# Kernel tuning notes

Hardware: AMD Instinct MI355X
Metric: run time of the kernel (lower is better)

## Reference

```python
import math
import jax, jax.numpy as jnp
import numpy as np

L, B = 576, 16           # residues, batch
HID, ALPHA = 800, 60     # lstm hidden, alphabet size
IN0, IN1 = 41, 2 * HID   # lstm layer input sizes (20 one-hot + 21 pssm)


def _unit(v):
    return v / jnp.linalg.norm(v, axis=-1, keepdims=True)


def _frame(a, b, c):
    # rotation matrix (columns) of the local reference frame at point c
    bc = _unit(c - b)
    n = _unit(jnp.cross(b - a, bc))
    return jnp.stack([bc, jnp.cross(n, bc), n], axis=-1)  # (..., 3, 3)


def _extend(a, b, c, ct):
    # place next atom given previous three atoms and SRF coordinates ct
    R = _frame(a, b, c)
    return c + jnp.einsum('...ij,...j->...i', R, ct)


def lstm_dir(x, w_ih, w_hh, b_ih, b_hh, reverse=False):
    # single-direction LSTM over x: (T, B, D); torch gate order i,f,g,o
    H = w_hh.shape[1]
    Bb = x.shape[1]

    def step(carry, xt):
        h, cst = carry
        gates = xt @ w_ih.T + b_ih + h @ w_hh.T + b_hh
        i, f, g, o = jnp.split(gates, 4, axis=-1)
        cnew = jax.nn.sigmoid(f) * cst + jax.nn.sigmoid(i) * jnp.tanh(g)
        hnew = jax.nn.sigmoid(o) * jnp.tanh(cnew)
        return (hnew, cnew), hnew

    zeros = jnp.zeros((Bb, H), x.dtype)
    _, hs = jax.lax.scan(step, (zeros, zeros), x, reverse=reverse)
    return hs  # (T, B, H), in original time order for both directions


def torsion_to_srf(r, theta, phi):
    # r, theta: (3,) fixed bond lengths/angles; phi: (L, B, 3) torsions
    r = r[None, None, :]
    th = theta[None, None, :]
    c = jnp.stack([r * jnp.cos(th) * jnp.ones_like(phi),
                   r * jnp.cos(phi) * jnp.sin(th),
                   r * jnp.sin(phi) * jnp.sin(th)], axis=-1)  # (L, B, 3, 3)
    Lx, Bx = phi.shape[0], phi.shape[1]
    return jnp.transpose(c, (0, 2, 1, 3)).reshape(3 * Lx, Bx, 3)


def pnerf(c_tilde, nfrag):
    # parallel NeRF: run nfrag fragments in parallel, then stitch sequentially
    A, Bb, _ = c_tilde.shape
    F = A // nfrag  # assumes divisibility (guaranteed by chosen L)
    c = c_tilde.reshape(nfrag, F, Bb, 3).transpose(1, 0, 2, 3).reshape(F, nfrag * Bb, 3)
    init = jnp.array([[-np.sqrt(0.5), np.sqrt(1.5), 0.0],
                      [-np.sqrt(2.0), 0.0, 0.0],
                      [0.0, 0.0, 0.0]], dtype=c_tilde.dtype)
    a0 = jnp.broadcast_to(init[0], (nfrag * Bb, 3))
    b0 = jnp.broadcast_to(init[1], (nfrag * Bb, 3))
    c0 = jnp.broadcast_to(init[2], (nfrag * Bb, 3))

    def step(carry, ct):
        a, b, cc = carry
        d = _extend(a, b, cc, ct)
        return (b, cc, d), d

    _, frag = jax.lax.scan(step, (a0, b0, c0), c)  # (F, nfrag*Bb, 3)
    frag = frag.reshape(F, nfrag, Bb, 3)

    coords = frag[:, 0]  # fragment 0 already in global frame
    for k in range(1, nfrag):  # small fixed loop over fragments
        R = _frame(coords[-3], coords[-2], coords[-1])  # (Bb, 3, 3)
        g = coords[-1][None] + jnp.einsum('bij,fbj->fbi', R, frag[:, k])
        coords = jnp.concatenate([coords, g], axis=0)
    return coords  # (3L, B, 3)


def _p(k, shape):
    return 0.05 * jax.random.normal(k, shape, dtype=jnp.float32)


def setup_inputs():
    key = jax.random.key(0)
    ks = jax.random.split(key, 32)
    inp = {}
    inp['seq'] = jax.random.randint(ks[0], (L, B), 0, 20)
    inp['pssm'] = jax.random.uniform(ks[1], (L, B, 21), dtype=jnp.float32)
    inp['length'] = jnp.full((B,), L, dtype=jnp.int32)  # full lengths (packing is a no-op)
    i = 2
    for layer, din in ((0, IN0), (1, IN1)):
        for d in ('f', 'b'):
            inp[f'w_ih_l{layer}{d}'] = _p(ks[i], (4 * HID, din)); i += 1
            inp[f'w_hh_l{layer}{d}'] = _p(ks[i], (4 * HID, HID)); i += 1
            inp[f'b_ih_l{layer}{d}'] = _p(ks[i], (4 * HID,)); i += 1
            inp[f'b_hh_l{layer}{d}'] = _p(ks[i], (4 * HID,)); i += 1
    inp['fc_w'] = _p(ks[i], (ALPHA, 2 * HID)); i += 1
    inp['fc_b'] = _p(ks[i], (ALPHA,)); i += 1
    inp['alphabet'] = jax.random.uniform(ks[i], (ALPHA, 3), minval=-math.pi, maxval=math.pi, dtype=jnp.float32); i += 1
    inp['bond_lengths'] = jnp.array([145.867432, 152.534744, 132.935516], dtype=jnp.float32)
    inp['bond_angles'] = jnp.array([1.019982, 1.20471, 1.109421], dtype=jnp.float32)
    return inp


def reference(seq, pssm, length,
              w_ih_l0f, w_hh_l0f, b_ih_l0f, b_hh_l0f,
              w_ih_l0b, w_hh_l0b, b_ih_l0b, b_hh_l0b,
              w_ih_l1f, w_hh_l1f, b_ih_l1f, b_hh_l1f,
              w_ih_l1b, w_hh_l1b, b_ih_l1b, b_hh_l1b,
              fc_w, fc_b, alphabet, bond_lengths, bond_angles):
    # eval mode: inter-layer dropout omitted; all lengths == L so packing is identity
    x = jnp.concatenate([jax.nn.one_hot(seq, 20, dtype=pssm.dtype), pssm], axis=-1)  # (L,B,41)
    h = jnp.concatenate([lstm_dir(x, w_ih_l0f, w_hh_l0f, b_ih_l0f, b_hh_l0f),
                         lstm_dir(x, w_ih_l0b, w_hh_l0b, b_ih_l0b, b_hh_l0b, reverse=True)], axis=-1)
    h = jnp.concatenate([lstm_dir(h, w_ih_l1f, w_hh_l1f, b_ih_l1f, b_hh_l1f),
                         lstm_dir(h, w_ih_l1b, w_hh_l1b, b_ih_l1b, b_hh_l1b, reverse=True)], axis=-1)
    p = jax.nn.softmax(h @ fc_w.T + fc_b, axis=-1)            # (L,B,ALPHA)
    phi = jnp.arctan2(p @ jnp.sin(alphabet), p @ jnp.cos(alphabet))  # (L,B,3)
    srf = torsion_to_srf(bond_lengths, bond_angles, phi)      # (3L,B,3)
    return pnerf(srf, int(math.sqrt(L)))                      # (3L,B,3)
```

## Files before the change

kernel.cpp:

```cpp
#include <hip/hip_runtime.h>
#include <hip/hip_fp16.h>

#define L_SEQ 576
#define BATCH 16
#define HIDDEN 800
#define NT 200
#define KQ_HH 25
#define KQ_L1 50
#define KQ_L0 2

typedef _Float16 h8 __attribute__((ext_vector_type(8)));
typedef _Float16 h4 __attribute__((ext_vector_type(4)));
typedef float f4 __attribute__((ext_vector_type(4)));
typedef int v4i __attribute__((ext_vector_type(4)));
typedef int v2i __attribute__((ext_vector_type(2)));

__device__ __forceinline__ float sigmoidf_(float x){
  x = fminf(30.f, fmaxf(-30.f, x));
  return 1.f/(1.f+__expf(-x));
}
__device__ __forceinline__ float tanhf_(float x){
  x = fminf(15.f, fmaxf(-15.f, x));
  float e = __expf(2.f*x);
  return (e-1.f)/(e+1.f);
}

__global__ void init_h(v4i* __restrict__ h){
  size_t i = (size_t)blockIdx.x*256 + threadIdx.x;
  v4i s = {0x7C007C00, 0x7C007C00, 0x7C007C00, 0x7C007C00};
  h[i] = s;
}

__global__ void build_x(const int* __restrict__ seq, const float* __restrict__ pssm,
                        _Float16* __restrict__ x){
  int i = blockIdx.x*256 + threadIdx.x;
  if(i >= L_SEQ*BATCH*64) return;
  int m = i >> 6, k = i & 63;
  float v = 0.f;
  if(k < 20)      v = (seq[m]==k) ? 1.f : 0.f;
  else if(k < 41) v = pssm[m*21 + (k-20)];
  x[i] = (_Float16)v;
}

__global__ void prep_w(
  const float* __restrict__ whh0f, const float* __restrict__ whh0b,
  const float* __restrict__ whh1f, const float* __restrict__ whh1b,
  const float* __restrict__ wih1f, const float* __restrict__ wih1b,
  const float* __restrict__ wih0f, const float* __restrict__ wih0b,
  h8* __restrict__ wp_hh, h8* __restrict__ wp1, h8* __restrict__ wp0)
{
  long idx = (long)blockIdx.x*256 + threadIdx.x;
  const long J1 = 4L*320000, J2 = 2L*640000, J3 = 2L*25600;
  if(idx < J1){
    int d = (int)(idx/320000); int r = (int)(idx%320000);
    int T = r/1600, q = (r%1600)/64, l = r&63;
    const float* W = (d==0)?whh0f:(d==1)?whh0b:(d==2)?whh1f:whh1b;
    int c = l&15; int n = (c&3)*800 + T*4 + (c>>2);
    const float* src = W + (size_t)n*800 + q*32 + ((l>>4)<<3);
    h8 v;
    #pragma unroll
    for(int j=0;j<8;++j) v[j] = (_Float16)src[j];
    wp_hh[idx] = v;
  } else if(idx < J1+J2){
    long i2 = idx - J1;
    int d = (int)(i2/640000); int r = (int)(i2%640000);
    int T = r/3200, q = (r%3200)/64, l = r&63;
    const float* W = d ? wih1b : wih1f;
    int c = l&15; int n = (c&3)*800 + T*4 + (c>>2);
    const float* src = W + (size_t)n*1600 + q*32 + ((l>>4)<<3);
    h8 v;
    #pragma unroll
    for(int j=0;j<8;++j) v[j] = (_Float16)src[j];
    wp1[i2] = v;
  } else if(idx < J1+J2+J3){
    long i3 = idx - J1 - J2;
    int d = (int)(i3/25600); int r = (int)(i3%25600);
    int T = r/128, q = (r%128)/64, l = r&63;
    const float* W = d ? wih0b : wih0f;
    int c = l&15; int n = (c&3)*800 + T*4 + (c>>2);
    int k0 = q*32 + ((l>>4)<<3);
    h8 v;
    #pragma unroll
    for(int j=0;j<8;++j){ int k = k0+j; v[j] = (_Float16)((k<41)? W[(size_t)n*41+k] : 0.f); }
    wp0[i3] = v;
  }
}

__global__ __launch_bounds__(256) void gemm_l0(
  const _Float16* __restrict__ A,
  const h8* __restrict__ WpF, const h8* __restrict__ WpB,
  const float* __restrict__ bihF, const float* __restrict__ bhhF,
  const float* __restrict__ bihB, const float* __restrict__ bhhB,
  _Float16* __restrict__ GpF, _Float16* __restrict__ GpB)
{
  const int wv = threadIdx.x >> 6;
  const int l  = threadIdx.x & 63;
  const int mg = blockIdx.x % 144;
  const int tg = blockIdx.x / 144;
  const int mt = mg*4 + wv;
  const int dir = tg / 50;
  const int Tb  = (tg % 50) * 4;
  const h8* Wp = dir ? WpB : WpF;
  const float* bih = dir ? bihB : bihF;
  const float* bhh = dir ? bhhB : bhhF;
  _Float16* Gp = dir ? GpB : GpF;

  const _Float16* ab = A + (size_t)(mt*16 + (l&15))*64 + ((l>>4)<<3);
  f4 acc[4] = {{0.f,0.f,0.f,0.f},{0.f,0.f,0.f,0.f},{0.f,0.f,0.f,0.f},{0.f,0.f,0.f,0.f}};
  for(int q=0;q<KQ_L0;++q){
    h8 av = *(const h8*)(ab + q*32);
    #pragma unroll
    for(int j=0;j<4;++j){
      h8 bv = Wp[((size_t)(Tb+j)*KQ_L0 + q)*64 + l];
      acc[j] = __builtin_amdgcn_mfma_f32_16x16x32_f16(bv, av, acc[j], 0, 0, 0);
    }
  }
  const int hi = l >> 4;
  #pragma unroll
  for(int j=0;j<4;++j){
    int T = Tb + j;
    int u = T*4 + hi;
    h4 o;
    #pragma unroll
    for(int r=0;r<4;++r){
      float bias = bih[r*800+u] + bhh[r*800+u];
      o[r] = (_Float16)(acc[j][r] + bias);
    }
    *(h4*)(Gp + (((size_t)mt*NT + T)*64 + l)*4) = o;
  }
}

__global__ __launch_bounds__(512) void gemm_l1(
  const h8* __restrict__ Af,
  const h8* __restrict__ WpF, const h8* __restrict__ WpB,
  const float* __restrict__ bihF, const float* __restrict__ bhhF,
  const float* __restrict__ bihB, const float* __restrict__ bhhB,
  _Float16* __restrict__ GpF, _Float16* __restrict__ GpB)
{
  __shared__ v4i ldsW[2][512];
  const int tid = threadIdx.x;
  const int wv = tid >> 6;
  const int l  = tid & 63;
  const int mg  = blockIdx.x % 36;
  const int tgd = blockIdx.x / 36;
  const int dir = tgd / 25;
  const int tg  = tgd % 25;
  const int Tb  = tg * 8;
  const int mt0 = mg*16 + wv*2;
  const h8* Wp = dir ? WpB : WpF;
  const float* bih = dir ? bihB : bihF;
  const float* bhh = dir ? bhhB : bhhF;
  _Float16* Gp = dir ? GpB : GpF;

  const h8* a0 = Af + (size_t)(mt0+0)*3200 + l;
  const h8* a1 = Af + (size_t)(mt0+1)*3200 + l;

  f4 acc[2][8];
  #pragma unroll
  for(int m=0;m<2;++m)
    #pragma unroll
    for(int j=0;j<8;++j){ acc[m][j][0]=0.f; acc[m][j][1]=0.f; acc[m][j][2]=0.f; acc[m][j][3]=0.f; }

  {
    int j = tid >> 6, ll = tid & 63;
    ldsW[0][tid] = *(const v4i*)(Wp + ((size_t)(Tb+j)*KQ_L1 + 0)*64 + ll);
  }
  h8 av0 = a0[0], av1 = a1[0];
  __syncthreads();
  for(int q=0;q<KQ_L1;++q){
    const int buf = q & 1;
    const int qn = (q+1 < KQ_L1) ? q+1 : q;
    if(q+1 < KQ_L1){
      int j = tid >> 6, ll = tid & 63;
      ldsW[buf^1][tid] = *(const v4i*)(Wp + ((size_t)(Tb+j)*KQ_L1 + (q+1))*64 + ll);
    }
    h8 an0 = a0[qn*64], an1 = a1[qn*64];
    #pragma unroll
    for(int j=0;j<8;++j){
      h8 bv = __builtin_bit_cast(h8, ldsW[buf][j*64 + l]);
      acc[0][j] = __builtin_amdgcn_mfma_f32_16x16x32_f16(bv, av0, acc[0][j], 0, 0, 0);
      acc[1][j] = __builtin_amdgcn_mfma_f32_16x16x32_f16(bv, av1, acc[1][j], 0, 0, 0);
    }
    __syncthreads();
    av0 = an0; av1 = an1;
  }
  const int hi = l >> 4;
  #pragma unroll
  for(int j=0;j<8;++j){
    int T = Tb + j;
    int u = T*4 + hi;
    float b0 = bih[0*800+u] + bhh[0*800+u];
    float b1 = bih[1*800+u] + bhh[1*800+u];
    float b2 = bih[2*800+u] + bhh[2*800+u];
    float b3 = bih[3*800+u] + bhh[3*800+u];
    #pragma unroll
    for(int m=0;m<2;++m){
      h4 o;
      o[0]=(_Float16)(acc[m][j][0]+b0); o[1]=(_Float16)(acc[m][j][1]+b1);
      o[2]=(_Float16)(acc[m][j][2]+b2); o[3]=(_Float16)(acc[m][j][3]+b3);
      *(h4*)(Gp + (((size_t)(mt0+m)*NT + T)*64 + l)*4) = o;
    }
  }
}

__global__ __launch_bounds__(256,1) void lstm_kernel(
  const h8* __restrict__ WpF, const h8* __restrict__ WpB,
  const _Float16* __restrict__ GpF, const _Float16* __restrict__ GpB,
  h8* __restrict__ hfrag)
{
  __shared__ __attribute__((aligned(16))) char lds_h[2*25600];
  const int tid = threadIdx.x;
  const int wv  = tid >> 6;
  const int l   = tid & 63;
  const bool bwd = blockIdx.x >= 50;
  const int T = ((bwd ? (int)blockIdx.x - 50 : (int)blockIdx.x) << 2) + wv;
  const h8* Wp = bwd ? WpB : WpF;
  const _Float16* Gp = bwd ? GpB : GpF;
  const int dirOff = bwd ? 1600 : 0;

  h8 Bf[KQ_HH];
  #pragma unroll
  for(int q=0;q<KQ_HH;++q) Bf[q] = Wp[(T*KQ_HH + q)*64 + l];

  float cs = 0.f;
  const int qb = wv*6;
  const int storeUnit = ((T>>3)<<6) + (((T>>1)&3)<<4);
  const int storeHalf = (T&1)<<3;

  for(int s=0; s<L_SEQ; ++s){
    const int t = bwd ? (L_SEQ-1-s) : s;

    h4 gp4 = *(const h4*)(Gp + (((size_t)t*NT + T)*64 + l)*4);

    #pragma unroll
    for(int q=0;q<KQ_HH;++q) asm volatile("" : "+v"(Bf[q]));

    char* lbuf = lds_h + (s&1)*25600;
    if(s > 0){
      const h8* src = hfrag + (size_t)(bwd ? t+1 : t-1)*3200 + dirOff + l;
      v4i w[7];
      for(;;){
        #pragma unroll
        for(int i=0;i<7;++i){
          unsigned long long ad = (unsigned long long)(src + (qb+i)*64);
          asm volatile("global_load_dwordx4 %0, %1, off sc1"
                       : "=v"(w[i]) : "v"(ad) : "memory");
        }
        asm volatile("s_waitcnt vmcnt(0)"
          : "+v"(w[0]),"+v"(w[1]),"+v"(w[2]),"+v"(w[3]),"+v"(w[4]),
            "+v"(w[5]),"+v"(w[6])
          :
          : "memory");
        int orac = 0;
        #pragma unroll
        for(int i=0;i<7;++i) orac |= (w[i][0]|w[i][1]) | (w[i][2]|w[i][3]);
        if(__all((orac & 0x40004000) == 0)) break;
        __builtin_amdgcn_s_sleep(1);
      }
      #pragma unroll
      for(int i=0;i<7;++i)
        *(v4i*)(lbuf + (qb+i)*1024 + l*16) = w[i];
    }
    __syncthreads();

    f4 acc[4];
    acc[0][0]=(float)gp4[0]; acc[0][1]=(float)gp4[1]; acc[0][2]=(float)gp4[2]; acc[0][3]=(float)gp4[3];
    #pragma unroll
    for(int j=1;j<4;++j){ acc[j][0]=0.f; acc[j][1]=0.f; acc[j][2]=0.f; acc[j][3]=0.f; }
    if(s > 0){
      #pragma unroll
      for(int q=0;q<KQ_HH;++q){
        v4i wq = *(const v4i*)(lbuf + q*1024 + l*16);
        acc[q&3] = __builtin_amdgcn_mfma_f32_16x16x32_f16(
                     Bf[q], __builtin_bit_cast(h8, wq), acc[q&3], 0,0,0);
      }
    }
    f4 g = (acc[0]+acc[1]) + (acc[2]+acc[3]);

    float cn = sigmoidf_(g[1])*cs + sigmoidf_(g[0])*tanhf_(g[2]);
    cs = cn;
    float hv = sigmoidf_(g[3])*tanhf_(cn);

    {
      _Float16 hf = (_Float16)hv;
      unsigned int u0 = (unsigned int)__builtin_bit_cast(unsigned short, hf);
      unsigned int up = (unsigned int)__shfl_xor((int)u0, 16, 64);
      unsigned int d01 = u0 | (up << 16);
      unsigned int d23 = (unsigned int)__shfl_xor((int)d01, 32, 64);
      if(l < 16){
        v2i ov; ov[0] = (int)d01; ov[1] = (int)d23;
        unsigned long long ad = (unsigned long long)
          ((char*)(hfrag + (size_t)t*3200 + dirOff + storeUnit + l) + storeHalf);
        asm volatile("global_store_dwordx2 %0, %1, off sc1" : : "v"(ad), "v"(ov) : "memory");
      }
    }
  }
}

__global__ void head_kernel(const h8* __restrict__ h1f,
                            const float* __restrict__ fcw, const float* __restrict__ fcb,
                            const float* __restrict__ alphabet,
                            const float* __restrict__ bl, const float* __restrict__ ba,
                            float* __restrict__ srf)
{
  __shared__ h8 sh8[16*201];
  __shared__ float slog[960];
  __shared__ float smax[16];
  __shared__ float sphi[48];
  const int t = blockIdx.x, tid = threadIdx.x;
  const h8* src = h1f + (size_t)t*3200;
  for(int u=tid; u<3200; u+=256){
    int q2 = u >> 6, r = u & 63, sub = r >> 4, m = r & 15;
    sh8[m*201 + (q2<<2) + sub] = src[u];
  }
  __syncthreads();
  for(int it=tid; it<960; it+=256){
    int j = it >> 4, b = it & 15;
    float acc = fcb[j];
    const float4* wr = (const float4*)(fcw + (size_t)j*1600);
    const h8* hr = sh8 + b*201;
    for(int k=0;k<200;++k){
      h8 hv = hr[k];
      float4 w0 = wr[2*k], w1 = wr[2*k+1];
      acc += w0.x*(float)hv[0] + w0.y*(float)hv[1] + w0.z*(float)hv[2] + w0.w*(float)hv[3]
           + w1.x*(float)hv[4] + w1.y*(float)hv[5] + w1.z*(float)hv[6] + w1.w*(float)hv[7];
    }
    slog[b*60 + j] = acc;
  }
  __syncthreads();
  if(tid < 16){
    float mx = -1e30f;
    for(int j=0;j<60;++j) mx = fmaxf(mx, slog[tid*60+j]);
    smax[tid] = mx;
  }
  __syncthreads();
  if(tid < 48){
    int b = tid/3, ax = tid%3;
    float s=0.f, c=0.f, mx = smax[b];
    for(int j=0;j<60;++j){
      float e = __expf(slog[b*60+j] - mx);
      float al = alphabet[j*3 + ax];
      s += e*__sinf(al); c += e*__cosf(al);
    }
    sphi[b*3+ax] = atan2f(s, c);
  }
  __syncthreads();
  if(tid < 144){
    int jj = tid/48; int r_ = tid%48; int b = r_/3, ax = r_%3;
    float rr = bl[jj], th = ba[jj], ph = sphi[b*3+jj];
    float v = (ax==0) ? rr*__cosf(th)
            : (ax==1) ? rr*__cosf(ph)*__sinf(th)
                      : rr*__sinf(ph)*__sinf(th);
    srf[(((size_t)(3*t+jj))*16 + b)*3 + ax] = v;
  }
}

__device__ __forceinline__ void frame_cols(
  float ax,float ay,float az, float bx,float by,float bz, float cx,float cy,float cz,
  float* R)
{
  float ux=cx-bx, uy=cy-by, uz=cz-bz;
  float ir = rsqrtf(ux*ux+uy*uy+uz*uz);
  float bcx=ux*ir, bcy=uy*ir, bcz=uz*ir;
  float px=bx-ax, py=by-ay, pz=bz-az;
  float nx=py*bcz-pz*bcy, ny=pz*bcx-px*bcz, nz=px*bcy-py*bcx;
  float in_ = rsqrtf(nx*nx+ny*ny+nz*nz);
  nx*=in_; ny*=in_; nz*=in_;
  float mx=ny*bcz-nz*bcy, my=nz*bcx-nx*bcz, mz=nx*bcy-ny*bcx;
  R[0]=bcx;R[1]=bcy;R[2]=bcz; R[3]=mx;R[4]=my;R[5]=mz; R[6]=nx;R[7]=ny;R[8]=nz;
}

__global__ void pnerf_kernel(const float* __restrict__ srf,
                             float* __restrict__ frag, float* __restrict__ out)
{
  __shared__ float tail[3][16][3];
  __shared__ float sR[16][9];
  __shared__ float sorg[16][3];
  const int tid = threadIdx.x;
  if(tid < 384){
    int k = tid >> 4, b = tid & 15;
    float ax=-0.70710678f, ay=1.22474487f, az=0.f;
    float bx=-1.41421356f, by=0.f, bz=0.f;
    float cx=0.f, cy=0.f, cz=0.f;
    for(int f=0; f<72; ++f){
      const float* ct = srf + (((size_t)(k*72+f))*16 + b)*3;
      float t0=ct[0], t1=ct[1], t2=ct[2];
      float R[9];
      frame_cols(ax,ay,az, bx,by,bz, cx,cy,cz, R);
      float dx = cx + R[0]*t0 + R[3]*t1 + R[6]*t2;
      float dy = cy + R[1]*t0 + R[4]*t1 + R[7]*t2;
      float dz = cz + R[2]*t0 + R[5]*t1 + R[8]*t2;
      float* fr = frag + (((size_t)(f*24+k))*16 + b)*3;
      fr[0]=dx; fr[1]=dy; fr[2]=dz;
      if(k == 0){
        float* o = out + ((size_t)(f*16)+b)*3;
        o[0]=dx; o[1]=dy; o[2]=dz;
        if(f >= 69){ tail[f-69][b][0]=dx; tail[f-69][b][1]=dy; tail[f-69][b][2]=dz; }
      }
      ax=bx; ay=by; az=bz;  bx=cx; by=cy; bz=cz;  cx=dx; cy=dy; cz=dz;
    }
  }
  __syncthreads();
  for(int kk=1; kk<24; ++kk){
    if(tid < 16){
      int b = tid;
      frame_cols(tail[0][b][0],tail[0][b][1],tail[0][b][2],
                 tail[1][b][0],tail[1][b][1],tail[1][b][2],
                 tail[2][b][0],tail[2][b][1],tail[2][b][2], &sR[b][0]);
      sorg[b][0]=tail[2][b][0]; sorg[b][1]=tail[2][b][1]; sorg[b][2]=tail[2][b][2];
    }
    __syncthreads();
    for(int idx=tid; idx<1152; idx+=blockDim.x){
      int f = idx >> 4, b = idx & 15;
      const float* v = frag + (((size_t)(f*24+kk))*16 + b)*3;
      float vx=v[0], vy=v[1], vz=v[2];
      float gx = sorg[b][0] + sR[b][0]*vx + sR[b][3]*vy + sR[b][6]*vz;
      float gy = sorg[b][1] + sR[b][1]*vx + sR[b][4]*vy + sR[b][7]*vz;
      float gz = sorg[b][2] + sR[b][2]*vx + sR[b][5]*vy + sR[b][8]*vz;
      float* o = out + (((size_t)(kk*72+f))*16 + b)*3;
      o[0]=gx; o[1]=gy; o[2]=gz;
      if(f >= 69){ tail[f-69][b][0]=gx; tail[f-69][b][1]=gy; tail[f-69][b][2]=gz; }
    }
    __syncthreads();
  }
}

extern "C" void kernel_launch(void* const* d_in, const int* in_sizes, int n_in,
                              void* d_out, int out_size, void* d_ws, size_t ws_size,
                              hipStream_t stream)
{
  (void)in_sizes; (void)n_in; (void)out_size; (void)ws_size;
  const int*   seq  = (const int*)d_in[0];
  const float* pssm = (const float*)d_in[1];
  const float* w_ih_l0f=(const float*)d_in[3];  const float* w_hh_l0f=(const float*)d_in[4];
  const float* b_ih_l0f=(const float*)d_in[5];  const float* b_hh_l0f=(const float*)d_in[6];
  const float* w_ih_l0b=(const float*)d_in[7];  const float* w_hh_l0b=(const float*)d_in[8];
  const float* b_ih_l0b=(const float*)d_in[9];  const float* b_hh_l0b=(const float*)d_in[10];
  const float* w_ih_l1f=(const float*)d_in[11]; const float* w_hh_l1f=(const float*)d_in[12];
  const float* b_ih_l1f=(const float*)d_in[13]; const float* b_hh_l1f=(const float*)d_in[14];
  const float* w_ih_l1b=(const float*)d_in[15]; const float* w_hh_l1b=(const float*)d_in[16];
  const float* b_ih_l1b=(const float*)d_in[17]; const float* b_hh_l1b=(const float*)d_in[18];
  const float* fc_w=(const float*)d_in[19];     const float* fc_b=(const float*)d_in[20];
  const float* alphabet=(const float*)d_in[21];
  const float* bl=(const float*)d_in[22];       const float* ba=(const float*)d_in[23];
  float* out = (float*)d_out;

  char* ws = (char*)d_ws;
  size_t o = 0;
  auto alloc = [&](size_t bytes){ size_t r = o; o = (o + bytes + 255) & ~(size_t)255; return r; };
  size_t o_wphh = alloc(4ull*320000*16);
  size_t o_wp1  = alloc(2ull*640000*16);
  size_t o_wp0  = alloc(2ull*25600*16);
  size_t o_gpf  = alloc(2ull*29491200);
  size_t o_gpb  = alloc(2ull*29491200);
  size_t o_h0   = alloc(16ull*576*3200);
  size_t o_h1   = alloc(16ull*576*3200);
  size_t o_x    = alloc(2ull*589824);
  size_t o_srf  = alloc(4ull*82944);
  size_t o_frag = alloc(4ull*82944);

  h8* wp_hh = (h8*)(ws + o_wphh);
  h8* wp1   = (h8*)(ws + o_wp1);
  h8* wp0   = (h8*)(ws + o_wp0);
  _Float16* gpf = (_Float16*)(ws + o_gpf);
  _Float16* gpb = (_Float16*)(ws + o_gpb);
  h8* h0    = (h8*)(ws + o_h0);
  h8* h1    = (h8*)(ws + o_h1);
  _Float16* x = (_Float16*)(ws + o_x);
  float* srf    = (float*)(ws + o_srf);
  float* frag   = (float*)(ws + o_frag);

  init_h<<<14400, 256, 0, stream>>>((v4i*)(ws + o_h0));
  build_x<<<2304, 256, 0, stream>>>(seq, pssm, x);
  prep_w<<<10200, 256, 0, stream>>>(w_hh_l0f, w_hh_l0b, w_hh_l1f, w_hh_l1b,
                                    w_ih_l1f, w_ih_l1b, w_ih_l0f, w_ih_l0b,
                                    wp_hh, wp1, wp0);
  gemm_l0<<<14400, 256, 0, stream>>>(x, wp0, wp0 + 25600,
                                     b_ih_l0f, b_hh_l0f, b_ih_l0b, b_hh_l0b, gpf, gpb);
  lstm_kernel<<<100, 256, 0, stream>>>(wp_hh, wp_hh + 320000, gpf, gpb, h0);
  gemm_l1<<<1800, 512, 0, stream>>>(h0, wp1, wp1 + 640000,
                                    b_ih_l1f, b_hh_l1f, b_ih_l1b, b_hh_l1b, gpf, gpb);
  lstm_kernel<<<100, 256, 0, stream>>>(wp_hh + 640000, wp_hh + 960000, gpf, gpb, h1);
  head_kernel<<<576, 256, 0, stream>>>(h1, fc_w, fc_b, alphabet, bl, ba, srf);
  pnerf_kernel<<<1, 512, 0, stream>>>(srf, frag, out);
}
```

Before: 2.794 ms.

## Fuse layer-1 input GEMM with recurrent LSTM via flag-polled producer/consumer blocks

Merges the layer-1 input-projection GEMM and the layer-1 recurrent LSTM into one persistent launch. The first 100 blocks run the recurrence and spin on NaN/Inf sentinel values in the gate buffer, which init_h fills before launch. The remaining blocks compute GEMM tiles in time order, with the backward direction reversed, so the recurrence can start before the whole GEMM is done. This hides GEMM time behind the serial recurrence, but it relies on co-residency of the recurrent blocks and on sentinel polling. It also adds an extra fill pass over the gate buffers.

```diff
diff --git a/kernel.cpp b/kernel.cpp
--- a/kernel.cpp
+++ b/kernel.cpp
@@ -127,79 +127,6 @@
       o[r] = (_Float16)(acc[j][r] + bias);
     }
     *(h4*)(Gp + (((size_t)mt*NT + T)*64 + l)*4) = o;
-  }
-}
-
-__global__ __launch_bounds__(512) void gemm_l1(
-  const h8* __restrict__ Af,
-  const h8* __restrict__ WpF, const h8* __restrict__ WpB,
-  const float* __restrict__ bihF, const float* __restrict__ bhhF,
-  const float* __restrict__ bihB, const float* __restrict__ bhhB,
-  _Float16* __restrict__ GpF, _Float16* __restrict__ GpB)
-{
-  __shared__ v4i ldsW[2][512];
-  const int tid = threadIdx.x;
-  const int wv = tid >> 6;
-  const int l  = tid & 63;
-  const int mg  = blockIdx.x % 36;
-  const int tgd = blockIdx.x / 36;
-  const int dir = tgd / 25;
-  const int tg  = tgd % 25;
-  const int Tb  = tg * 8;
-  const int mt0 = mg*16 + wv*2;
-  const h8* Wp = dir ? WpB : WpF;
-  const float* bih = dir ? bihB : bihF;
-  const float* bhh = dir ? bhhB : bhhF;
-  _Float16* Gp = dir ? GpB : GpF;
-
-  const h8* a0 = Af + (size_t)(mt0+0)*3200 + l;
-  const h8* a1 = Af + (size_t)(mt0+1)*3200 + l;
-
-  f4 acc[2][8];
-  #pragma unroll
-  for(int m=0;m<2;++m)
-    #pragma unroll
-    for(int j=0;j<8;++j){ acc[m][j][0]=0.f; acc[m][j][1]=0.f; acc[m][j][2]=0.f; acc[m][j][3]=0.f; }
-
-  {
-    int j = tid >> 6, ll = tid & 63;
-    ldsW[0][tid] = *(const v4i*)(Wp + ((size_t)(Tb+j)*KQ_L1 + 0)*64 + ll);
-  }
-  h8 av0 = a0[0], av1 = a1[0];
-  __syncthreads();
-  for(int q=0;q<KQ_L1;++q){
-    const int buf = q & 1;
-    const int qn = (q+1 < KQ_L1) ? q+1 : q;
-    if(q+1 < KQ_L1){
-      int j = tid >> 6, ll = tid & 63;
-      ldsW[buf^1][tid] = *(const v4i*)(Wp + ((size_t)(Tb+j)*KQ_L1 + (q+1))*64 + ll);
-    }
-    h8 an0 = a0[qn*64], an1 = a1[qn*64];
-    #pragma unroll
-    for(int j=0;j<8;++j){
-      h8 bv = __builtin_bit_cast(h8, ldsW[buf][j*64 + l]);
-      acc[0][j] = __builtin_amdgcn_mfma_f32_16x16x32_f16(bv, av0, acc[0][j], 0, 0, 0);
-      acc[1][j] = __builtin_amdgcn_mfma_f32_16x16x32_f16(bv, av1, acc[1][j], 0, 0, 0);
-    }
-    __syncthreads();
-    av0 = an0; av1 = an1;
-  }
-  const int hi = l >> 4;
-  #pragma unroll
-  for(int j=0;j<8;++j){
-    int T = Tb + j;
-    int u = T*4 + hi;
-    float b0 = bih[0*800+u] + bhh[0*800+u];
-    float b1 = bih[1*800+u] + bhh[1*800+u];
-    float b2 = bih[2*800+u] + bhh[2*800+u];
-    float b3 = bih[3*800+u] + bhh[3*800+u];
-    #pragma unroll
-    for(int m=0;m<2;++m){
-      h4 o;
-      o[0]=(_Float16)(acc[m][j][0]+b0); o[1]=(_Float16)(acc[m][j][1]+b1);
-      o[2]=(_Float16)(acc[m][j][2]+b2); o[3]=(_Float16)(acc[m][j][3]+b3);
-      *(h4*)(Gp + (((size_t)(mt0+m)*NT + T)*64 + l)*4) = o;
-    }
   }
 }
 
@@ -291,6 +218,194 @@
         v2i ov; ov[0] = (int)d01; ov[1] = (int)d23;
         unsigned long long ad = (unsigned long long)
           ((char*)(hfrag + (size_t)t*3200 + dirOff + storeUnit + l) + storeHalf);
+        asm volatile("global_store_dwordx2 %0, %1, off sc1" : : "v"(ad), "v"(ov) : "memory");
+      }
+    }
+  }
+}
+
+__global__ __launch_bounds__(512,1) void fused_l1(
+  const h8* __restrict__ WhF, const h8* __restrict__ WhB,
+  _Float16* __restrict__ GpF, _Float16* __restrict__ GpB,
+  h8* __restrict__ hfrag,
+  const h8* __restrict__ Af,
+  const h8* __restrict__ W1F, const h8* __restrict__ W1B,
+  const float* __restrict__ bihF, const float* __restrict__ bhhF,
+  const float* __restrict__ bihB, const float* __restrict__ bhhB)
+{
+  __shared__ __attribute__((aligned(16))) char smem[2*25600];
+  const int tid = threadIdx.x;
+  if(blockIdx.x < 100){
+    const bool act = tid < 256;
+    const int wv = (tid >> 6) & 3;
+    const int l  = tid & 63;
+    const bool bwd = blockIdx.x >= 50;
+    const int T = ((bwd ? (int)blockIdx.x - 50 : (int)blockIdx.x) << 2) + wv;
+    const h8* Wp = bwd ? WhB : WhF;
+    const _Float16* Gp = bwd ? GpB : GpF;
+    const int dirOff = bwd ? 1600 : 0;
+
+    h8 Bf[KQ_HH];
+    if(act){
+      #pragma unroll
+      for(int q=0;q<KQ_HH;++q) Bf[q] = Wp[(T*KQ_HH + q)*64 + l];
+    }
+    float cs = 0.f;
+    const int qb = wv*6;
+    const int storeUnit = ((T>>3)<<6) + (((T>>1)&3)<<4);
+    const int storeHalf = (T&1)<<3;
+
+    for(int s=0; s<L_SEQ; ++s){
+      const int t = bwd ? (L_SEQ-1-s) : s;
+      v2i gpw;
+      char* lbuf = smem + (s&1)*25600;
+      unsigned long long gpad = 0;
+      if(act){
+        gpad = (unsigned long long)(Gp + (((size_t)t*NT + T)*64 + l)*4);
+        asm volatile("global_load_dwordx2 %0, %1, off sc1"
+                     : "=v"(gpw) : "v"(gpad) : "memory");
+        #pragma unroll
+        for(int q=0;q<KQ_HH;++q) asm volatile("" : "+v"(Bf[q]));
+        if(s > 0){
+          const h8* src = hfrag + (size_t)(bwd ? t+1 : t-1)*3200 + dirOff + l;
+          v4i w[7];
+          for(;;){
+            #pragma unroll
+            for(int i=0;i<7;++i){
+              unsigned long long ad = (unsigned long long)(src + (qb+i)*64);
+              asm volatile("global_load_dwordx4 %0, %1, off sc1"
+                           : "=v"(w[i]) : "v"(ad) : "memory");
+            }
+            asm volatile("s_waitcnt vmcnt(0)"
+              : "+v"(w[0]),"+v"(w[1]),"+v"(w[2]),"+v"(w[3]),"+v"(w[4]),
+                "+v"(w[5]),"+v"(w[6])
+              :
+              : "memory");
+            int orac = 0;
+            #pragma unroll
+            for(int i=0;i<7;++i) orac |= (w[i][0]|w[i][1]) | (w[i][2]|w[i][3]);
+            if(__all((orac & 0x40004000) == 0)) break;
+            __builtin_amdgcn_s_sleep(1);
+          }
+          #pragma unroll
+          for(int i=0;i<7;++i)
+            *(v4i*)(lbuf + (qb+i)*1024 + l*16) = w[i];
+        }
+      }
+      __syncthreads();
+      if(act){
+        for(;;){
+          asm volatile("s_waitcnt vmcnt(0)" : "+v"(gpw) : : "memory");
+          int lo = gpw[0], hi = gpw[1];
+          int na = (((lo & 0x7C00) == 0x7C00) ? 1 : 0)
+                 | ((((lo>>16) & 0x7C00) == 0x7C00) ? 1 : 0)
+                 | (((hi & 0x7C00) == 0x7C00) ? 1 : 0)
+                 | ((((hi>>16) & 0x7C00) == 0x7C00) ? 1 : 0);
+          if(__all(na == 0)) break;
+          __builtin_amdgcn_s_sleep(1);
+          asm volatile("global_load_dwordx2 %0, %1, off sc1"
+                       : "=v"(gpw) : "v"(gpad) : "memory");
+        }
+        h4 gp4 = __builtin_bit_cast(h4, gpw);
+
+        f4 acc[4];
+        acc[0][0]=(float)gp4[0]; acc[0][1]=(float)gp4[1]; acc[0][2]=(float)gp4[2]; acc[0][3]=(float)gp4[3];
+        #pragma unroll
+        for(int j=1;j<4;++j){ acc[j][0]=0.f; acc[j][1]=0.f; acc[j][2]=0.f; acc[j][3]=0.f; }
+        if(s > 0){
+          #pragma unroll
+          for(int q=0;q<KQ_HH;++q){
+            v4i wq = *(const v4i*)(lbuf + q*1024 + l*16);
+            acc[q&3] = __builtin_amdgcn_mfma_f32_16x16x32_f16(
+                         Bf[q], __builtin_bit_cast(h8, wq), acc[q&3], 0,0,0);
+          }
+        }
+        f4 g = (acc[0]+acc[1]) + (acc[2]+acc[3]);
+
+        float cn = sigmoidf_(g[1])*cs + sigmoidf_(g[0])*tanhf_(g[2]);
+        cs = cn;
+        float hv = sigmoidf_(g[3])*tanhf_(cn);
+
+        _Float16 hf = (_Float16)hv;
+        unsigned int u0 = (unsigned int)__builtin_bit_cast(unsigned short, hf);
+        unsigned int up = (unsigned int)__shfl_xor((int)u0, 16, 64);
+        unsigned int d01 = u0 | (up << 16);
+        unsigned int d23 = (unsigned int)__shfl_xor((int)d01, 32, 64);
+        if(l < 16){
+          v2i ov; ov[0] = (int)d01; ov[1] = (int)d23;
+          unsigned long long ad = (unsigned long long)
+            ((char*)(hfrag + (size_t)t*3200 + dirOff + storeUnit + l) + storeHalf);
+          asm volatile("global_store_dwordx2 %0, %1, off sc1" : : "v"(ad), "v"(ov) : "memory");
+        }
+      }
+    }
+  } else {
+    v4i (*ldsW)[512] = (v4i(*)[512])smem;
+    const int wv = tid >> 6;
+    const int l  = tid & 63;
+    const int g  = (int)blockIdx.x - 100;
+    const int dir = g & 1;
+    const int p   = g >> 1;
+    const int mgs = p / 25;
+    const int tg  = p % 25;
+    if(mgs >= 36) return;
+    const int mg = dir ? (35 - mgs) : mgs;
+    const int Tb = tg * 8;
+    const int mt0 = mg*16 + wv*2;
+    const h8* Wp = dir ? W1B : W1F;
+    const float* bih = dir ? bihB : bihF;
+    const float* bhh = dir ? bhhB : bhhF;
+    _Float16* Gp = dir ? GpB : GpF;
+
+    const h8* a0 = Af + (size_t)(mt0+0)*3200 + l;
+    const h8* a1 = Af + (size_t)(mt0+1)*3200 + l;
+
+    f4 acc[2][8];
+    #pragma unroll
+    for(int m=0;m<2;++m)
+      #pragma unroll
+      for(int j=0;j<8;++j){ acc[m][j][0]=0.f; acc[m][j][1]=0.f; acc[m][j][2]=0.f; acc[m][j][3]=0.f; }
+
+    {
+      int j = tid >> 6, ll = tid & 63;
+      ldsW[0][tid] = *(const v4i*)(Wp + ((size_t)(Tb+j)*KQ_L1 + 0)*64 + ll);
+    }
+    h8 av0 = a0[0], av1 = a1[0];
+    __syncthreads();
+    for(int q=0;q<KQ_L1;++q){
+      const int buf = q & 1;
+      const int qn = (q+1 < KQ_L1) ? q+1 : q;
+      if(q+1 < KQ_L1){
+        int j = tid >> 6, ll = tid & 63;
+        ldsW[buf^1][tid] = *(const v4i*)(Wp + ((size_t)(Tb+j)*KQ_L1 + (q+1))*64 + ll);
+      }
+      h8 an0 = a0[qn*64], an1 = a1[qn*64];
+      #pragma unroll
+      for(int j=0;j<8;++j){
+        h8 bv = __builtin_bit_cast(h8, ldsW[buf][j*64 + l]);
+        acc[0][j] = __builtin_amdgcn_mfma_f32_16x16x32_f16(bv, av0, acc[0][j], 0, 0, 0);
+        acc[1][j] = __builtin_amdgcn_mfma_f32_16x16x32_f16(bv, av1, acc[1][j], 0, 0, 0);
+      }
+      __syncthreads();
+      av0 = an0; av1 = an1;
+    }
+    const int hi = l >> 4;
+    #pragma unroll
+    for(int j=0;j<8;++j){
+      int T = Tb + j;
+      int u = T*4 + hi;
+      float b0 = bih[0*800+u] + bhh[0*800+u];
+      float b1 = bih[1*800+u] + bhh[1*800+u];
+      float b2 = bih[2*800+u] + bhh[2*800+u];
+      float b3 = bih[3*800+u] + bhh[3*800+u];
+      #pragma unroll
+      for(int m=0;m<2;++m){
+        h4 o;
+        o[0]=(_Float16)(acc[m][j][0]+b0); o[1]=(_Float16)(acc[m][j][1]+b1);
+        o[2]=(_Float16)(acc[m][j][2]+b2); o[3]=(_Float16)(acc[m][j][3]+b3);
+        v2i ov = __builtin_bit_cast(v2i, o);
+        unsigned long long ad = (unsigned long long)
+          (Gp + (((size_t)(mt0+m)*NT + T)*64 + l)*4);
         asm volatile("global_store_dwordx2 %0, %1, off sc1" : : "v"(ad), "v"(ov) : "memory");
       }
     }
@@ -478,9 +593,11 @@
   gemm_l0<<<14400, 256, 0, stream>>>(x, wp0, wp0 + 25600,
                                      b_ih_l0f, b_hh_l0f, b_ih_l0b, b_hh_l0b, gpf, gpb);
   lstm_kernel<<<100, 256, 0, stream>>>(wp_hh, wp_hh + 320000, gpf, gpb, h0);
-  gemm_l1<<<1800, 512, 0, stream>>>(h0, wp1, wp1 + 640000,
-                                    b_ih_l1f, b_hh_l1f, b_ih_l1b, b_hh_l1b, gpf, gpb);
-  lstm_kernel<<<100, 256, 0, stream>>>(wp_hh + 640000, wp_hh + 960000, gpf, gpb, h1);
+  init_h<<<28800, 256, 0, stream>>>((v4i*)(ws + o_gpf));
+  fused_l1<<<2100, 512, 0, stream>>>(wp_hh + 640000, wp_hh + 960000,
+                                     gpf, gpb, h1, h0,
+                                     wp1, wp1 + 640000,
+                                     b_ih_l1f, b_hh_l1f, b_ih_l1b, b_hh_l1b);
   head_kernel<<<576, 256, 0, stream>>>(h1, fc_w, fc_b, alphabet, bl, ba, srf);
   pnerf_kernel<<<1, 512, 0, stream>>>(srf, frag, out);
 }
```

Result: faster. 2.717 ms (-2.8%).
